# Optimization experiments

Measured on AMD Instinct MI355X. Metric: run time of the kernel, lower is better.

The kernel has to match this reference:

```python
import jax, jax.numpy as jnp
import numpy as np
from jax import lax

EPS = 1e-6
TANH_CLIP = 1.0 - 1e-5
FRECHET_ITERS = 10


def _sqnorm(x):
    return jnp.sum(x * x, axis=-1, keepdims=True)


def _norm(x):
    return jnp.sqrt(jnp.clip(_sqnorm(x), EPS))


def _lambda(x, c):
    # conformal factor lambda_x = 2 / (1 - c ||x||^2)
    return 2.0 / jnp.clip(1.0 - c * _sqnorm(x), EPS)


def mobius_add(x, y, c):
    x2 = _sqnorm(x)
    y2 = _sqnorm(y)
    xy = jnp.sum(x * y, axis=-1, keepdims=True)
    num = (1.0 + 2.0 * c * xy + c * y2) * x + (1.0 - c * x2) * y
    den = 1.0 + 2.0 * c * xy + (c * c) * x2 * y2
    return num / jnp.clip(den, EPS)


def expmap(x, u, c):
    sc = jnp.sqrt(c)
    un = _norm(u)
    second = jnp.tanh(sc * _lambda(x, c) * un / 2.0) * u / (sc * un)
    return mobius_add(x, second, c)


def logmap(x, y, c):
    sc = jnp.sqrt(c)
    m = mobius_add(-x, y, c)
    mn = _norm(m)
    t = jnp.arctanh(jnp.clip(sc * mn, 0.0, TANH_CLIP))
    return (2.0 / (sc * _lambda(x, c))) * t * m / mn


def exp0(u, c):
    sc = jnp.sqrt(c)
    un = _norm(u)
    return jnp.tanh(sc * un) * u / (sc * un)


def dist(x, y, c):
    sc = jnp.sqrt(c)
    mn = _norm(mobius_add(-x, y, c))
    return (2.0 / sc) * jnp.arctanh(jnp.clip(sc * mn, 0.0, TANH_CLIP))[..., 0]


def gyr(a, b, w, c):
    # gyr[a,b]w = -(a (+) b) (+) (a (+) (b (+) w))
    return mobius_add(-mobius_add(a, b, c), mobius_add(a, mobius_add(b, w, c), c), c)


def transp(x, y, u, c):
    # parallel transport x -> y:  (lam_x / lam_y) * gyr[y, -x] u
    return (_lambda(x, c) / _lambda(y, c)) * gyr(y, -x, u, c)


def frechet_mean(x, c):
    # Karcher fixed-point iteration: mu <- exp_mu(mean_i log_mu(x_i))
    m = jnp.mean(x, axis=0)  # (D,)
    max_norm = (1.0 - 1e-3) / jnp.sqrt(c)
    mn = _norm(m)[0]
    m = m * jnp.minimum(1.0, max_norm / mn)

    def step(mu, _):
        g = jnp.mean(logmap(mu, x, c), axis=0)
        return expmap(mu, g, c), None

    mu, _ = lax.scan(step, m, None, length=FRECHET_ITERS)
    return mu


def setup_inputs() -> dict:
    key = jax.random.key(0)
    k1, k2 = jax.random.split(key)
    B, S, D = 64, 256, 256
    K = jnp.float32(-1.2)
    sc = np.sqrt(1.2)
    x = jax.random.normal(k1, (B, S, D), dtype=jnp.float32)
    # project points strictly inside the Poincare ball of radius 1/sqrt(c)
    x = x / (1.0 + _norm(x)) * jnp.float32(0.7 / sc)
    mean_param = 0.01 * jax.random.normal(k2, (D,), dtype=jnp.float32)
    var_param = jnp.float32(1.0)
    return {"x": x, "K": K, "mean_param": mean_param, "var_param": var_param}


def reference(x, K, mean_param, var_param):
    c = -K  # positive ball curvature (K = -1.2)
    shapes = x.shape
    xf = x.reshape(-1, shapes[-1])  # (N, D)
    on_manifold = exp0(mean_param, c)          # (D,) target mean on manifold
    mu = frechet_mean(xf, c)                   # (D,) batch Frechet mean
    var = jnp.mean(dist(xf, mu, c) ** 2)       # Frechet variance (scalar)
    logm = transp(mu, on_manifold, logmap(mu, xf, c), c)  # (N, D)
    logm = jnp.sqrt(var_param / (var + 1e-6)) * logm
    out = expmap(on_manifold, logm, c)         # (N, D)
    return out.reshape(shapes)
```

## Files before the change

kernel.cpp:

```cpp
#include <hip/hip_runtime.h>
#include <math.h>
#include <string.h>

#define EPSF 1e-6f
#define TCLIP (1.0f - 1e-5f)
#define NPTS 16384
#define DDIM 256
#define NBLK 128
#define NTHR 1024
#define PPB 128
#define NWAVE 16
#define PPW 8
#define PSTR 260
#define FRECHET_ITERS_N 10

#define WS_PA 64
#define WS_PB (WS_PA + NBLK * PSTR)

__device__ __forceinline__ void st_pair_sc1(float* addr, float a, float b) {
    float2 f2 = make_float2(a, b);
    double dv; memcpy(&dv, &f2, 8);
    __hip_atomic_store((double*)addr, dv, __ATOMIC_RELAXED, __HIP_MEMORY_SCOPE_AGENT);
}
__device__ __forceinline__ float2 ld_pair_sc1(const float* addr) {
    double dv = __hip_atomic_load((const double*)addr, __ATOMIC_RELAXED, __HIP_MEMORY_SCOPE_AGENT);
    float2 f2; memcpy(&f2, &dv, 8);
    return f2;
}
__device__ __forceinline__ void st_f_sc1(float* addr, float v) {
    __hip_atomic_store(addr, v, __ATOMIC_RELAXED, __HIP_MEMORY_SCOPE_AGENT);
}
__device__ __forceinline__ void st_u_sc1(unsigned* addr, unsigned v) {
    __hip_atomic_store(addr, v, __ATOMIC_RELAXED, __HIP_MEMORY_SCOPE_AGENT);
}
__device__ __forceinline__ unsigned ld_u_sc1(const unsigned* addr) {
    return __hip_atomic_load(addr, __ATOMIC_RELAXED, __HIP_MEMORY_SCOPE_AGENT);
}

__device__ __forceinline__ float block_sum(float v) {
    __shared__ float s_bs[NWAVE];
    #pragma unroll
    for (int off = 32; off; off >>= 1) v += __shfl_xor(v, off);
    const int w = threadIdx.x >> 6, l = threadIdx.x & 63;
    __syncthreads();
    if (l == 0) s_bs[w] = v;
    __syncthreads();
    float s = 0.f;
    #pragma unroll
    for (int i = 0; i < NWAVE; ++i) s += s_bs[i];
    return s;
}

__device__ __forceinline__ void block_sum2(float& a, float& b) {
    __shared__ float sa2[NWAVE], sb2[NWAVE];
    #pragma unroll
    for (int off = 32; off; off >>= 1) { a += __shfl_xor(a, off); b += __shfl_xor(b, off); }
    const int w = threadIdx.x >> 6, l = threadIdx.x & 63;
    __syncthreads();
    if (l == 0) { sa2[w] = a; sb2[w] = b; }
    __syncthreads();
    a = 0.f; b = 0.f;
    #pragma unroll
    for (int i = 0; i < NWAVE; ++i) { a += sa2[i]; b += sb2[i]; }
}

__device__ __forceinline__ void block_sum3(float& a, float& b, float& cc) {
    __shared__ float sa3[NWAVE], sb3[NWAVE], sc3[NWAVE];
    #pragma unroll
    for (int off = 32; off; off >>= 1) {
        a += __shfl_xor(a, off); b += __shfl_xor(b, off); cc += __shfl_xor(cc, off);
    }
    const int w = threadIdx.x >> 6, l = threadIdx.x & 63;
    __syncthreads();
    if (l == 0) { sa3[w] = a; sb3[w] = b; sc3[w] = cc; }
    __syncthreads();
    a = 0.f; b = 0.f; cc = 0.f;
    #pragma unroll
    for (int i = 0; i < NWAVE; ++i) { a += sa3[i]; b += sb3[i]; cc += sc3[i]; }
}

__global__ void init_tags(float* ws) {
    int t = threadIdx.x;
    if (t < NBLK) {
        st_u_sc1((unsigned*)(ws + WS_PA + t * PSTR + 258), 0u);
        st_u_sc1((unsigned*)(ws + WS_PB + t * PSTR + 258), 0u);
    }
}

__global__ __launch_bounds__(NTHR, 1) void rbn_fused(
    const float* __restrict__ x, const float* __restrict__ Kp,
    const float* __restrict__ mean_param, const float* __restrict__ var_param,
    float* __restrict__ out, float* __restrict__ ws)
{
    const float c = -Kp[0];
    const float sc = sqrtf(c);
    const float N1 = 1.f / NPTS;
    const int t = threadIdx.x, lane = t & 63, wv = t >> 6;
    const int b = blockIdx.x;
    const int p0 = b * PPB;
    const float4* xr = ((const float4*)x) + p0 * 64;

    float* PA = ws + WS_PA;
    float* PB = ws + WS_PB;

    __shared__ float mu_s[DDIM], om_s[DDIM], g_s[DDIM];
    __shared__ float dpart[PPB * 65];
    __shared__ float dqr[PPB * 9];
    __shared__ float y2_s[PPB], e_s[PPB], d_s[PPB], w_s[PPB], sA_s[PPB], fx_s[PPB];
    __shared__ float pseg[NWAVE * DDIM];

    unsigned barno = 0;

    float4 xreg[PPW];
    #pragma unroll
    for (int i = 0; i < PPW; ++i)
        xreg[i] = xr[(wv * PPW + i) * 64 + lane];

    auto dot_rows = [&](float4 v4, float* dst, bool self) {
        #pragma unroll
        for (int i = 0; i < PPW; ++i) {
            float4 xv = xreg[i];
            float4 u4 = self ? xv : v4;
            dpart[(wv * PPW + i) * 65 + lane] =
                xv.x * u4.x + xv.y * u4.y + xv.z * u4.z + xv.w * u4.w;
        }
        __syncthreads();
        {
            int pl = t & 127, q = t >> 7;
            float s = 0.f;
            #pragma unroll
            for (int j = 0; j < 8; ++j) s += dpart[pl * 65 + q * 8 + j];
            dqr[pl * 9 + q] = s;
        }
        __syncthreads();
        if (t < PPB) {
            float s = 0.f;
            #pragma unroll
            for (int j = 0; j < 8; ++j) s += dqr[t * 9 + j];
            dst[t] = s;
        }
        __syncthreads();
    };

    auto wsum_rows = [&](const float* wgt, float* dstv) {
        float4 a = make_float4(0.f, 0.f, 0.f, 0.f);
        #pragma unroll
        for (int i = 0; i < PPW; ++i) {
            float w = wgt ? wgt[wv * PPW + i] : 1.f;
            a.x += w * xreg[i].x; a.y += w * xreg[i].y;
            a.z += w * xreg[i].z; a.w += w * xreg[i].w;
        }
        __syncthreads();
        ((float4*)(pseg + wv * DDIM))[lane] = a;
        __syncthreads();
        float s = 0.f;
        if (t < DDIM) {
            #pragma unroll
            for (int w = 0; w < NWAVE; ++w) s += pseg[w * DDIM + t];
        }
        float partner = __shfl_xor(s, 1);
        if (t < DDIM && !(t & 1))
            st_pair_sc1(dstv + t, s, partner);
    };

    auto publish = [&](float* buf) {
        __syncthreads();
        if (t == 0) st_u_sc1((unsigned*)(buf + b * PSTR + 258), barno);
    };
    auto wait_tags = [&](const float* buf) {
        if (t < NBLK) {
            const unsigned* tg = (const unsigned*)(buf + t * PSTR + 258);
            while (ld_u_sc1(tg) < barno)
                __builtin_amdgcn_s_sleep(1);
        }
        __syncthreads();
    };

    auto reduce128 = [&](const float* buf, float* dstv) {
        const int dg = t & 127, sg = t >> 7;
        float ax = 0.f, ay = 0.f;
        #pragma unroll
        for (int j = 0; j < 16; ++j) {
            float2 v = ld_pair_sc1(buf + (sg * 16 + j) * PSTR + 2 * dg);
            ax += v.x; ay += v.y;
        }
        __syncthreads();
        ((float2*)(pseg + sg * DDIM))[dg] = make_float2(ax, ay);
        __syncthreads();
        if (t < DDIM) {
            float s = 0.f;
            #pragma unroll
            for (int w = 0; w < 8; ++w) s += pseg[w * DDIM + t];
            dstv[t] = s;
        }
    };

    {
        float u = (t < DDIM) ? mean_param[t] : 0.f;
        float un2 = block_sum(u * u);
        float un = sqrtf(fmaxf(un2, EPSF));
        if (t < DDIM) om_s[t] = tanhf(sc * un) * u / (sc * un);
    }
    float om2;
    { float v = (t < DDIM) ? om_s[t] * om_s[t] : 0.f; om2 = block_sum(v); }

    dot_rows(make_float4(0.f, 0.f, 0.f, 0.f), y2_s, true);
    {
        float4 om4 = ((const float4*)om_s)[lane];
        dot_rows(om4, e_s, false);
    }

    ++barno;
    wsum_rows(nullptr, PA + b * PSTR);
    publish(PA);
    wait_tags(PA);

    float mu2;
    {
        reduce128(PA, g_s);
        float m = (t < DDIM) ? g_s[t] * N1 : 0.f;
        float mn2 = block_sum(m * m);
        float mn = sqrtf(fmaxf(mn2, EPSF));
        float maxn = (1.f - 1e-3f) / sc;
        float f = fminf(1.f, maxn / mn);
        if (t < DDIM) mu_s[t] = m * f;
        mu2 = f * f * mn2;
        __syncthreads();
    }

    for (int it = 0; it < FRECHET_ITERS_N; ++it) {
        float* buf = (it & 1) ? PA : PB;
        ++barno;
        {
            float4 mu4 = ((const float4*)mu_s)[lane];
            dot_rows(mu4, d_s, false);
        }
        if (t < PPB) {
            float y2 = y2_s[t], d = d_s[t];
            float P = 1.f - 2.f * c * d;
            float den = fmaxf(P + c * c * mu2 * y2, EPSF);
            float A = -(P + c * y2) / den;
            float B = (1.f - c * mu2) / den;
            float mn2 = fmaxf(A * A * mu2 + 2.f * A * B * d + B * B * y2, EPSF);
            float mn = sqrtf(mn2);
            float tt = atanhf(fminf(sc * mn, TCLIP));
            float s = (fmaxf(1.f - c * mu2, EPSF) / sc) * tt / mn;
            w_s[t] = s * B;
            sA_s[t] = s * A;
        }
        __syncthreads();
        wsum_rows(w_s, buf + b * PSTR);
        float sAl = (t < PPB) ? sA_s[t] : 0.f;
        float wdl = (t < PPB) ? w_s[t] * d_s[t] : 0.f;
        block_sum2(sAl, wdl);
        if (t == 0) st_pair_sc1(buf + b * PSTR + 256, sAl, wdl);
        publish(buf);
        wait_tags(buf);

        reduce128(buf, g_s);
        float vv  = (t < DDIM) ? g_s[t] * g_s[t] : 0.f;
        float2 sp = make_float2(0.f, 0.f);
        if (t < NBLK) sp = ld_pair_sc1(buf + t * PSTR + 256);
        float sAt = sp.x, wdt = sp.y;
        block_sum3(vv, sAt, wdt);
        float gn2 = N1 * N1 * (vv + 2.f * sAt * wdt + sAt * sAt * mu2);
        float mg  = N1 * (wdt + sAt * mu2);
        float un = sqrtf(fmaxf(gn2, EPSF));
        float lam = 2.f / fmaxf(1.f - c * mu2, EPSF);
        float k = tanhf(sc * lam * un * 0.5f) / (sc * un);
        float ms = k * mg;
        float s2 = k * k * gn2;
        float aa = 1.f + 2.f * c * ms + c * s2;
        float bb2 = 1.f - c * mu2;
        float den = fmaxf(1.f + 2.f * c * ms + c * c * mu2 * s2, EPSF);
        float cm = (aa + bb2 * k * N1 * sAt) / den;
        float cv = (bb2 * k * N1) / den;
        if (t < DDIM) mu_s[t] = cm * mu_s[t] + cv * g_s[t];
        mu2 = cm * cm * mu2 + 2.f * cm * cv * wdt + cv * cv * vv;
        __syncthreads();
    }

    float* vbuf = ((FRECHET_ITERS_N - 1) & 1) ? PB : PA;
    ++barno;
    {
        float4 mu4 = ((const float4*)mu_s)[lane];
        dot_rows(mu4, d_s, false);
    }
    if (t < PPB) {
        float y2 = y2_s[t], d = d_s[t];
        float P = 1.f - 2.f * c * d;
        float den = fmaxf(P + c * c * mu2 * y2, EPSF);
        float A = -(P + c * y2) / den;
        float B = (1.f - c * mu2) / den;
        float mn2 = fmaxf(A * A * mu2 + 2.f * A * B * d + B * B * y2, EPSF);
        float mn = sqrtf(mn2);
        float tt = atanhf(fminf(sc * mn, TCLIP));
        float dd = (2.f / sc) * tt;
        sA_s[t] = dd * dd;
    }
    __syncthreads();
    {
        float v = (t < PPB) ? sA_s[t] : 0.f;
        float tot = block_sum(v);
        if (t == 0) st_f_sc1(vbuf + b * PSTR + 256, tot);
    }
    publish(vbuf);
    wait_tags(vbuf);

    float va = (t < NBLK) ? __hip_atomic_load(vbuf + t * PSTR + 256,
                 __ATOMIC_RELAXED, __HIP_MEMORY_SCOPE_AGENT) : 0.f;
    float ob = (t < DDIM) ? om_s[t] * mu_s[t] : 0.f;
    block_sum2(va, ob);
    float var = va * N1;
    float gamma = sqrtf(var_param[0] / (var + 1e-6f));
    float omu = ob;

    const float Amu = fmaxf(1.f - c * mu2, EPSF);
    const float Aom = fmaxf(1.f - c * om2, EPSF);
    const float ratio = Aom / Amu;
    const float aq = 1.f - 2.f * c * omu + c * mu2;
    const float bq = 1.f - c * om2;
    const float dqv = fmaxf(1.f - 2.f * c * omu + c * c * om2 * mu2, EPSF);
    const float qo = aq / dqv, qm = -bq / dqv;
    const float q2 = qo * qo * om2 + 2.f * qo * qm * omu + qm * qm * mu2;
    const float lam_om = 2.f / Aom;

    if (t < PPB) {
        float y2 = y2_s[t], d = d_s[t], e = e_s[t];
        auto dotOm3 = [&](float po, float pm, float px) { return po * om2 + pm * omu + px * e; };
        auto dotMu3 = [&](float po, float pm, float px) { return po * omu + pm * mu2 + px * d; };
        auto sqn3 = [&](float po, float pm, float px) {
            return po * po * om2 + pm * pm * mu2 + px * px * y2
                 + 2.f * (po * pm * omu + po * px * e + pm * px * d);
        };

        float P = 1.f - 2.f * c * d;
        float den0 = fmaxf(P + c * c * mu2 * y2, EPSF);
        float A = -(P + c * y2) / den0;
        float B = (1.f - c * mu2) / den0;
        float mn2 = fmaxf(A * A * mu2 + 2.f * A * B * d + B * B * y2, EPSF);
        float mn = sqrtf(mn2);
        float tt = atanhf(fminf(sc * mn, TCLIP));
        float s = (fmaxf(1.f - c * mu2, EPSF) / sc) * tt / mn;
        float Um = s * A, Ux = s * B;

        float xy1 = -dotMu3(0.f, Um, Ux);
        float Y21 = sqn3(0.f, Um, Ux);
        float a1 = 1.f + 2.f * c * xy1 + c * Y21;
        float b1 = 1.f - c * mu2;
        float dn1 = fmaxf(1.f + 2.f * c * xy1 + c * c * mu2 * Y21, EPSF);
        float h1m = (-a1 + b1 * Um) / dn1;
        float h1x = (b1 * Ux) / dn1;

        float xy2 = dotOm3(0.f, h1m, h1x);
        float Y22 = sqn3(0.f, h1m, h1x);
        float a2 = 1.f + 2.f * c * xy2 + c * Y22;
        float b2 = 1.f - c * om2;
        float dn2 = fmaxf(1.f + 2.f * c * xy2 + c * c * om2 * Y22, EPSF);
        float h2o = a2 / dn2;
        float h2m = (b2 * h1m) / dn2;
        float h2x = (b2 * h1x) / dn2;

        float xy3 = -(qo * dotOm3(h2o, h2m, h2x) + qm * dotMu3(h2o, h2m, h2x));
        float Y23 = sqn3(h2o, h2m, h2x);
        float a3 = 1.f + 2.f * c * xy3 + c * Y23;
        float b3 = 1.f - c * q2;
        float dn3 = fmaxf(1.f + 2.f * c * xy3 + c * c * q2 * Y23, EPSF);
        float g2o = (-a3 * qo + b3 * h2o) / dn3;
        float g2m = (-a3 * qm + b3 * h2m) / dn3;
        float g2x = (b3 * h2x) / dn3;

        float k1 = ratio * gamma;
        float Lo = k1 * g2o, Lm = k1 * g2m, Lx = k1 * g2x;
        float un2 = sqn3(Lo, Lm, Lx);
        float un = sqrtf(fmaxf(un2, EPSF));
        float coef = tanhf(sc * lam_om * un * 0.5f) / (sc * un);
        float So = coef * Lo, Sm = coef * Lm, Sx = coef * Lx;
        float xy4 = dotOm3(So, Sm, Sx);
        float Y24 = coef * coef * un2;
        float a4 = 1.f + 2.f * c * xy4 + c * Y24;
        float b4 = 1.f - c * om2;
        float dn4 = fmaxf(1.f + 2.f * c * xy4 + c * c * om2 * Y24, EPSF);
        w_s[t]  = (a4 + b4 * So) / dn4;
        sA_s[t] = (b4 * Sm) / dn4;
        fx_s[t] = (b4 * Sx) / dn4;
    }
    __syncthreads();

    {
        float4 mu4f = ((const float4*)mu_s)[lane];
        float4 om4f = ((const float4*)om_s)[lane];
        #pragma unroll
        for (int i = 0; i < PPW; ++i) {
            int pl = wv * PPW + i;
            float fo = w_s[pl], fm = sA_s[pl], fx = fx_s[pl];
            float4 x4 = xreg[i];
            float4 o4;
            o4.x = fo * om4f.x + fm * mu4f.x + fx * x4.x;
            o4.y = fo * om4f.y + fm * mu4f.y + fx * x4.y;
            o4.z = fo * om4f.z + fm * mu4f.z + fx * x4.z;
            o4.w = fo * om4f.w + fm * mu4f.w + fx * x4.w;
            ((float4*)out)[(p0 + pl) * 64 + lane] = o4;
        }
    }
}

extern "C" void kernel_launch(void* const* d_in, const int* in_sizes, int n_in,
                              void* d_out, int out_size, void* d_ws, size_t ws_size,
                              hipStream_t stream) {
    const float* x = (const float*)d_in[0];
    const float* K = (const float*)d_in[1];
    const float* mean_param = (const float*)d_in[2];
    const float* var_param = (const float*)d_in[3];
    float* out = (float*)d_out;
    float* ws = (float*)d_ws;

    init_tags<<<1, 256, 0, stream>>>(ws);
    void* args[] = {(void*)&x, (void*)&K, (void*)&mean_param, (void*)&var_param,
                    (void*)&out, (void*)&ws};
    hipLaunchCooperativeKernel((const void*)rbn_fused, dim3(NBLK), dim3(NTHR),
                               args, 0, stream);
}
```

Measured before the change: 205.8 us.

## Overlap grid-barrier waits with local work and trim block-level syncs

```diff
diff --git a/kernel.cpp b/kernel.cpp
--- a/kernel.cpp
+++ b/kernel.cpp
@@ -30,6 +30,9 @@
 __device__ __forceinline__ void st_f_sc1(float* addr, float v) {
     __hip_atomic_store(addr, v, __ATOMIC_RELAXED, __HIP_MEMORY_SCOPE_AGENT);
 }
+__device__ __forceinline__ float ld_f_sc1(const float* addr) {
+    return __hip_atomic_load(addr, __ATOMIC_RELAXED, __HIP_MEMORY_SCOPE_AGENT);
+}
 __device__ __forceinline__ void st_u_sc1(unsigned* addr, unsigned v) {
     __hip_atomic_store(addr, v, __ATOMIC_RELAXED, __HIP_MEMORY_SCOPE_AGENT);
 }
@@ -49,34 +52,6 @@
     #pragma unroll
     for (int i = 0; i < NWAVE; ++i) s += s_bs[i];
     return s;
-}
-
-__device__ __forceinline__ void block_sum2(float& a, float& b) {
-    __shared__ float sa2[NWAVE], sb2[NWAVE];
-    #pragma unroll
-    for (int off = 32; off; off >>= 1) { a += __shfl_xor(a, off); b += __shfl_xor(b, off); }
-    const int w = threadIdx.x >> 6, l = threadIdx.x & 63;
-    __syncthreads();
-    if (l == 0) { sa2[w] = a; sb2[w] = b; }
-    __syncthreads();
-    a = 0.f; b = 0.f;
-    #pragma unroll
-    for (int i = 0; i < NWAVE; ++i) { a += sa2[i]; b += sb2[i]; }
-}
-
-__device__ __forceinline__ void block_sum3(float& a, float& b, float& cc) {
-    __shared__ float sa3[NWAVE], sb3[NWAVE], sc3[NWAVE];
-    #pragma unroll
-    for (int off = 32; off; off >>= 1) {
-        a += __shfl_xor(a, off); b += __shfl_xor(b, off); cc += __shfl_xor(cc, off);
-    }
-    const int w = threadIdx.x >> 6, l = threadIdx.x & 63;
-    __syncthreads();
-    if (l == 0) { sa3[w] = a; sb3[w] = b; sc3[w] = cc; }
-    __syncthreads();
-    a = 0.f; b = 0.f; cc = 0.f;
-    #pragma unroll
-    for (int i = 0; i < NWAVE; ++i) { a += sa3[i]; b += sb3[i]; cc += sc3[i]; }
 }
 
 __global__ void init_tags(float* ws) {
@@ -103,11 +78,12 @@
     float* PA = ws + WS_PA;
     float* PB = ws + WS_PB;
 
-    __shared__ float mu_s[DDIM], om_s[DDIM], g_s[DDIM];
+    __shared__ float mu_s[DDIM], om_s[DDIM];
     __shared__ float dpart[PPB * 65];
     __shared__ float dqr[PPB * 9];
     __shared__ float y2_s[PPB], e_s[PPB], d_s[PPB], w_s[PPB], sA_s[PPB], fx_s[PPB];
     __shared__ float pseg[NWAVE * DDIM];
+    __shared__ float part1[NWAVE], part2[NWAVE], part3[NWAVE];
 
     unsigned barno = 0;
 
@@ -116,58 +92,7 @@
     for (int i = 0; i < PPW; ++i)
         xreg[i] = xr[(wv * PPW + i) * 64 + lane];
 
-    auto dot_rows = [&](float4 v4, float* dst, bool self) {
-        #pragma unroll
-        for (int i = 0; i < PPW; ++i) {
-            float4 xv = xreg[i];
-            float4 u4 = self ? xv : v4;
-            dpart[(wv * PPW + i) * 65 + lane] =
-                xv.x * u4.x + xv.y * u4.y + xv.z * u4.z + xv.w * u4.w;
-        }
-        __syncthreads();
-        {
-            int pl = t & 127, q = t >> 7;
-            float s = 0.f;
-            #pragma unroll
-            for (int j = 0; j < 8; ++j) s += dpart[pl * 65 + q * 8 + j];
-            dqr[pl * 9 + q] = s;
-        }
-        __syncthreads();
-        if (t < PPB) {
-            float s = 0.f;
-            #pragma unroll
-            for (int j = 0; j < 8; ++j) s += dqr[t * 9 + j];
-            dst[t] = s;
-        }
-        __syncthreads();
-    };
-
-    auto wsum_rows = [&](const float* wgt, float* dstv) {
-        float4 a = make_float4(0.f, 0.f, 0.f, 0.f);
-        #pragma unroll
-        for (int i = 0; i < PPW; ++i) {
-            float w = wgt ? wgt[wv * PPW + i] : 1.f;
-            a.x += w * xreg[i].x; a.y += w * xreg[i].y;
-            a.z += w * xreg[i].z; a.w += w * xreg[i].w;
-        }
-        __syncthreads();
-        ((float4*)(pseg + wv * DDIM))[lane] = a;
-        __syncthreads();
-        float s = 0.f;
-        if (t < DDIM) {
-            #pragma unroll
-            for (int w = 0; w < NWAVE; ++w) s += pseg[w * DDIM + t];
-        }
-        float partner = __shfl_xor(s, 1);
-        if (t < DDIM && !(t & 1))
-            st_pair_sc1(dstv + t, s, partner);
-    };
-
-    auto publish = [&](float* buf) {
-        __syncthreads();
-        if (t == 0) st_u_sc1((unsigned*)(buf + b * PSTR + 258), barno);
-    };
-    auto wait_tags = [&](const float* buf) {
+    auto poll_tags = [&](const float* buf) {
         if (t < NBLK) {
             const unsigned* tg = (const unsigned*)(buf + t * PSTR + 258);
             while (ld_u_sc1(tg) < barno)
@@ -176,25 +101,6 @@
         __syncthreads();
     };
 
-    auto reduce128 = [&](const float* buf, float* dstv) {
-        const int dg = t & 127, sg = t >> 7;
-        float ax = 0.f, ay = 0.f;
-        #pragma unroll
-        for (int j = 0; j < 16; ++j) {
-            float2 v = ld_pair_sc1(buf + (sg * 16 + j) * PSTR + 2 * dg);
-            ax += v.x; ay += v.y;
-        }
-        __syncthreads();
-        ((float2*)(pseg + sg * DDIM))[dg] = make_float2(ax, ay);
-        __syncthreads();
-        if (t < DDIM) {
-            float s = 0.f;
-            #pragma unroll
-            for (int w = 0; w < 8; ++w) s += pseg[w * DDIM + t];
-            dstv[t] = s;
-        }
-    };
-
     {
         float u = (t < DDIM) ? mean_param[t] : 0.f;
         float un2 = block_sum(u * u);
@@ -204,22 +110,90 @@
     float om2;
     { float v = (t < DDIM) ? om_s[t] * om_s[t] : 0.f; om2 = block_sum(v); }
 
-    dot_rows(make_float4(0.f, 0.f, 0.f, 0.f), y2_s, true);
-    {
+    ++barno;
+    {
+        float4 a = make_float4(0.f, 0.f, 0.f, 0.f);
+        #pragma unroll
+        for (int i = 0; i < PPW; ++i) {
+            a.x += xreg[i].x; a.y += xreg[i].y; a.z += xreg[i].z; a.w += xreg[i].w;
+        }
+        __syncthreads();
+        ((float4*)(pseg + wv * DDIM))[lane] = a;
+        __syncthreads();
+        float s = 0.f;
+        if (t < DDIM) {
+            #pragma unroll
+            for (int w = 0; w < NWAVE; ++w) s += pseg[w * DDIM + t];
+        }
+        float partner = __shfl_xor(s, 1);
+        if (t < DDIM && !(t & 1)) st_pair_sc1(PA + b * PSTR + t, s, partner);
+        __syncthreads();
+        if (t == 0) st_u_sc1((unsigned*)(PA + b * PSTR + 258), barno);
+    }
+    {
+        #pragma unroll
+        for (int i = 0; i < PPW; ++i) {
+            float4 xv = xreg[i];
+            dpart[(wv * PPW + i) * 65 + lane] =
+                xv.x * xv.x + xv.y * xv.y + xv.z * xv.z + xv.w * xv.w;
+        }
+        __syncthreads();
+        { int pl = t & 127, q = t >> 7; float s = 0.f;
+          #pragma unroll
+          for (int j = 0; j < 8; ++j) s += dpart[pl * 65 + q * 8 + j];
+          dqr[pl * 9 + q] = s; }
+        __syncthreads();
+        if (t < PPB) { float s = 0.f;
+            #pragma unroll
+            for (int j = 0; j < 8; ++j) s += dqr[t * 9 + j];
+            y2_s[t] = s; }
+        __syncthreads();
         float4 om4 = ((const float4*)om_s)[lane];
-        dot_rows(om4, e_s, false);
-    }
-
-    ++barno;
-    wsum_rows(nullptr, PA + b * PSTR);
-    publish(PA);
-    wait_tags(PA);
+        #pragma unroll
+        for (int i = 0; i < PPW; ++i) {
+            float4 xv = xreg[i];
+            dpart[(wv * PPW + i) * 65 + lane] =
+                xv.x * om4.x + xv.y * om4.y + xv.z * om4.z + xv.w * om4.w;
+        }
+        __syncthreads();
+        { int pl = t & 127, q = t >> 7; float s = 0.f;
+          #pragma unroll
+          for (int j = 0; j < 8; ++j) s += dpart[pl * 65 + q * 8 + j];
+          dqr[pl * 9 + q] = s; }
+        __syncthreads();
+        if (t < PPB) { float s = 0.f;
+            #pragma unroll
+            for (int j = 0; j < 8; ++j) s += dqr[t * 9 + j];
+            e_s[t] = s; }
+    }
+    poll_tags(PA);
 
     float mu2;
     {
-        reduce128(PA, g_s);
-        float m = (t < DDIM) ? g_s[t] * N1 : 0.f;
-        float mn2 = block_sum(m * m);
+        const int dg = t & 127, sg = t >> 7;
+        float ax = 0.f, ay = 0.f;
+        #pragma unroll
+        for (int j = 0; j < 16; ++j) {
+            float2 v = ld_pair_sc1(PA + (sg * 16 + j) * PSTR + 2 * dg);
+            ax += v.x; ay += v.y;
+        }
+        __syncthreads();
+        ((float2*)(pseg + sg * DDIM))[dg] = make_float2(ax, ay);
+        __syncthreads();
+        float m = 0.f, mm = 0.f;
+        if (t < DDIM) {
+            float s = 0.f;
+            #pragma unroll
+            for (int w = 0; w < 8; ++w) s += pseg[w * DDIM + t];
+            m = s * N1; mm = m * m;
+        }
+        #pragma unroll
+        for (int off = 32; off; off >>= 1) mm += __shfl_xor(mm, off);
+        if (lane == 0) part1[wv] = mm;
+        __syncthreads();
+        float mn2 = 0.f;
+        #pragma unroll
+        for (int i = 0; i < NWAVE; ++i) mn2 += part1[i];
         float mn = sqrtf(fmaxf(mn2, EPSF));
         float maxn = (1.f - 1e-3f) / sc;
         float f = fminf(1.f, maxn / mn);
@@ -231,12 +205,25 @@
     for (int it = 0; it < FRECHET_ITERS_N; ++it) {
         float* buf = (it & 1) ? PA : PB;
         ++barno;
-        {
-            float4 mu4 = ((const float4*)mu_s)[lane];
-            dot_rows(mu4, d_s, false);
-        }
+        float4 mu4 = ((const float4*)mu_s)[lane];
+        #pragma unroll
+        for (int i = 0; i < PPW; ++i) {
+            float4 xv = xreg[i];
+            dpart[(wv * PPW + i) * 65 + lane] =
+                xv.x * mu4.x + xv.y * mu4.y + xv.z * mu4.z + xv.w * mu4.w;
+        }
+        __syncthreads();
+        { int pl = t & 127, q = t >> 7; float s = 0.f;
+          #pragma unroll
+          for (int j = 0; j < 8; ++j) s += dpart[pl * 65 + q * 8 + j];
+          dqr[pl * 9 + q] = s; }
+        __syncthreads();
+        float sAv = 0.f, wdv = 0.f;
         if (t < PPB) {
-            float y2 = y2_s[t], d = d_s[t];
+            float d = 0.f;
+            #pragma unroll
+            for (int j = 0; j < 8; ++j) d += dqr[t * 9 + j];
+            float y2 = y2_s[t];
             float P = 1.f - 2.f * c * d;
             float den = fmaxf(P + c * c * mu2 * y2, EPSF);
             float A = -(P + c * y2) / den;
@@ -245,26 +232,75 @@
             float mn = sqrtf(mn2);
             float tt = atanhf(fminf(sc * mn, TCLIP));
             float s = (fmaxf(1.f - c * mu2, EPSF) / sc) * tt / mn;
-            w_s[t] = s * B;
-            sA_s[t] = s * A;
-        }
-        __syncthreads();
-        wsum_rows(w_s, buf + b * PSTR);
-        float sAl = (t < PPB) ? sA_s[t] : 0.f;
-        float wdl = (t < PPB) ? w_s[t] * d_s[t] : 0.f;
-        block_sum2(sAl, wdl);
-        if (t == 0) st_pair_sc1(buf + b * PSTR + 256, sAl, wdl);
-        publish(buf);
-        wait_tags(buf);
-
-        reduce128(buf, g_s);
-        float vv  = (t < DDIM) ? g_s[t] * g_s[t] : 0.f;
+            float w = s * B;
+            w_s[t] = w;
+            sAv = s * A;
+            wdv = w * d;
+        }
+        __syncthreads();
+        {
+            float4 a = make_float4(0.f, 0.f, 0.f, 0.f);
+            #pragma unroll
+            for (int i = 0; i < PPW; ++i) {
+                float w = w_s[wv * PPW + i];
+                a.x += w * xreg[i].x; a.y += w * xreg[i].y;
+                a.z += w * xreg[i].z; a.w += w * xreg[i].w;
+            }
+            ((float4*)(pseg + wv * DDIM))[lane] = a;
+            #pragma unroll
+            for (int off = 32; off; off >>= 1) {
+                sAv += __shfl_xor(sAv, off); wdv += __shfl_xor(wdv, off);
+            }
+            if (lane == 0) { part1[wv] = sAv; part2[wv] = wdv; }
+        }
+        __syncthreads();
+        {
+            float s = 0.f;
+            if (t < DDIM) {
+                #pragma unroll
+                for (int w = 0; w < NWAVE; ++w) s += pseg[w * DDIM + t];
+            }
+            float partner = __shfl_xor(s, 1);
+            if (t < DDIM && !(t & 1)) st_pair_sc1(buf + b * PSTR + t, s, partner);
+            if (t == 0) {
+                float sa = 0.f, wd = 0.f;
+                #pragma unroll
+                for (int i = 0; i < NWAVE; ++i) { sa += part1[i]; wd += part2[i]; }
+                st_pair_sc1(buf + b * PSTR + 256, sa, wd);
+            }
+        }
+        __syncthreads();
+        if (t == 0) st_u_sc1((unsigned*)(buf + b * PSTR + 258), barno);
+        poll_tags(buf);
+        const int dg = t & 127, sg = t >> 7;
+        float ax = 0.f, ay = 0.f;
+        #pragma unroll
+        for (int j = 0; j < 16; ++j) {
+            float2 v = ld_pair_sc1(buf + (sg * 16 + j) * PSTR + 2 * dg);
+            ax += v.x; ay += v.y;
+        }
         float2 sp = make_float2(0.f, 0.f);
         if (t < NBLK) sp = ld_pair_sc1(buf + t * PSTR + 256);
+        ((float2*)(pseg + sg * DDIM))[dg] = make_float2(ax, ay);
+        __syncthreads();
+        float g = 0.f, vvv = 0.f;
+        if (t < DDIM) {
+            #pragma unroll
+            for (int w = 0; w < 8; ++w) g += pseg[w * DDIM + t];
+            vvv = g * g;
+        }
         float sAt = sp.x, wdt = sp.y;
-        block_sum3(vv, sAt, wdt);
-        float gn2 = N1 * N1 * (vv + 2.f * sAt * wdt + sAt * sAt * mu2);
-        float mg  = N1 * (wdt + sAt * mu2);
+        #pragma unroll
+        for (int off = 32; off; off >>= 1) {
+            vvv += __shfl_xor(vvv, off); sAt += __shfl_xor(sAt, off); wdt += __shfl_xor(wdt, off);
+        }
+        if (lane == 0) { part1[wv] = vvv; part2[wv] = sAt; part3[wv] = wdt; }
+        __syncthreads();
+        float vv = 0.f, sa = 0.f, wd = 0.f;
+        #pragma unroll
+        for (int i = 0; i < NWAVE; ++i) { vv += part1[i]; sa += part2[i]; wd += part3[i]; }
+        float gn2 = N1 * N1 * (vv + 2.f * sa * wd + sa * sa * mu2);
+        float mg  = N1 * (wd + sa * mu2);
         float un = sqrtf(fmaxf(gn2, EPSF));
         float lam = 2.f / fmaxf(1.f - c * mu2, EPSF);
         float k = tanhf(sc * lam * un * 0.5f) / (sc * un);
@@ -273,10 +309,10 @@
         float aa = 1.f + 2.f * c * ms + c * s2;
         float bb2 = 1.f - c * mu2;
         float den = fmaxf(1.f + 2.f * c * ms + c * c * mu2 * s2, EPSF);
-        float cm = (aa + bb2 * k * N1 * sAt) / den;
+        float cm = (aa + bb2 * k * N1 * sa) / den;
         float cv = (bb2 * k * N1) / den;
-        if (t < DDIM) mu_s[t] = cm * mu_s[t] + cv * g_s[t];
-        mu2 = cm * cm * mu2 + 2.f * cm * cv * wdt + cv * cv * vv;
+        if (t < DDIM) mu_s[t] = cm * mu_s[t] + cv * g;
+        mu2 = cm * cm * mu2 + 2.f * cm * cv * wd + cv * cv * vv;
         __syncthreads();
     }
 
@@ -284,36 +320,54 @@
     ++barno;
     {
         float4 mu4 = ((const float4*)mu_s)[lane];
-        dot_rows(mu4, d_s, false);
-    }
-    if (t < PPB) {
-        float y2 = y2_s[t], d = d_s[t];
-        float P = 1.f - 2.f * c * d;
-        float den = fmaxf(P + c * c * mu2 * y2, EPSF);
-        float A = -(P + c * y2) / den;
-        float B = (1.f - c * mu2) / den;
-        float mn2 = fmaxf(A * A * mu2 + 2.f * A * B * d + B * B * y2, EPSF);
-        float mn = sqrtf(mn2);
-        float tt = atanhf(fminf(sc * mn, TCLIP));
-        float dd = (2.f / sc) * tt;
-        sA_s[t] = dd * dd;
-    }
-    __syncthreads();
-    {
-        float v = (t < PPB) ? sA_s[t] : 0.f;
-        float tot = block_sum(v);
-        if (t == 0) st_f_sc1(vbuf + b * PSTR + 256, tot);
-    }
-    publish(vbuf);
-    wait_tags(vbuf);
-
-    float va = (t < NBLK) ? __hip_atomic_load(vbuf + t * PSTR + 256,
-                 __ATOMIC_RELAXED, __HIP_MEMORY_SCOPE_AGENT) : 0.f;
-    float ob = (t < DDIM) ? om_s[t] * mu_s[t] : 0.f;
-    block_sum2(va, ob);
-    float var = va * N1;
-    float gamma = sqrtf(var_param[0] / (var + 1e-6f));
-    float omu = ob;
+        #pragma unroll
+        for (int i = 0; i < PPW; ++i) {
+            float4 xv = xreg[i];
+            dpart[(wv * PPW + i) * 65 + lane] =
+                xv.x * mu4.x + xv.y * mu4.y + xv.z * mu4.z + xv.w * mu4.w;
+        }
+        __syncthreads();
+        { int pl = t & 127, q = t >> 7; float s = 0.f;
+          #pragma unroll
+          for (int j = 0; j < 8; ++j) s += dpart[pl * 65 + q * 8 + j];
+          dqr[pl * 9 + q] = s; }
+        __syncthreads();
+        float vval = 0.f;
+        if (t < PPB) {
+            float d = 0.f;
+            #pragma unroll
+            for (int j = 0; j < 8; ++j) d += dqr[t * 9 + j];
+            d_s[t] = d;
+            float y2 = y2_s[t];
+            float P = 1.f - 2.f * c * d;
+            float den = fmaxf(P + c * c * mu2 * y2, EPSF);
+            float A = -(P + c * y2) / den;
+            float B = (1.f - c * mu2) / den;
+            float mn2 = fmaxf(A * A * mu2 + 2.f * A * B * d + B * B * y2, EPSF);
+            float mn = sqrtf(mn2);
+            float tt = atanhf(fminf(sc * mn, TCLIP));
+            float dd = (2.f / sc) * tt;
+            vval = dd * dd;
+        }
+        float ov = (t < DDIM) ? om_s[t] * mu_s[t] : 0.f;
+        #pragma unroll
+        for (int off = 32; off; off >>= 1) {
+            vval += __shfl_xor(vval, off); ov += __shfl_xor(ov, off);
+        }
+        if (lane == 0) { part1[wv] = vval; part2[wv] = ov; }
+        __syncthreads();
+        if (t == 0) {
+            float tot = 0.f;
+            #pragma unroll
+            for (int i = 0; i < NWAVE; ++i) tot += part1[i];
+            st_f_sc1(vbuf + b * PSTR + 256, tot);
+        }
+        __syncthreads();
+        if (t == 0) st_u_sc1((unsigned*)(vbuf + b * PSTR + 258), barno);
+    }
+    float omu = 0.f;
+    #pragma unroll
+    for (int i = 0; i < NWAVE; ++i) omu += part2[i];
 
     const float Amu = fmaxf(1.f - c * mu2, EPSF);
     const float Aom = fmaxf(1.f - c * om2, EPSF);
@@ -333,7 +387,6 @@
             return po * po * om2 + pm * pm * mu2 + px * px * y2
                  + 2.f * (po * pm * omu + po * px * e + pm * px * d);
         };
-
         float P = 1.f - 2.f * c * d;
         float den0 = fmaxf(P + c * c * mu2 * y2, EPSF);
         float A = -(P + c * y2) / den0;
@@ -366,17 +419,34 @@
         float a3 = 1.f + 2.f * c * xy3 + c * Y23;
         float b3 = 1.f - c * q2;
         float dn3 = fmaxf(1.f + 2.f * c * xy3 + c * c * q2 * Y23, EPSF);
-        float g2o = (-a3 * qo + b3 * h2o) / dn3;
-        float g2m = (-a3 * qm + b3 * h2m) / dn3;
-        float g2x = (b3 * h2x) / dn3;
-
+        w_s[t]  = (-a3 * qo + b3 * h2o) / dn3;
+        sA_s[t] = (-a3 * qm + b3 * h2m) / dn3;
+        fx_s[t] = (b3 * h2x) / dn3;
+    }
+    poll_tags(vbuf);
+
+    float va = (t < NBLK) ? ld_f_sc1(vbuf + t * PSTR + 256) : 0.f;
+    #pragma unroll
+    for (int off = 32; off; off >>= 1) va += __shfl_xor(va, off);
+    if (lane == 0) part1[wv] = va;
+    __syncthreads();
+    float vsum = 0.f;
+    #pragma unroll
+    for (int i = 0; i < NWAVE; ++i) vsum += part1[i];
+    float var = vsum * N1;
+    float gamma = sqrtf(var_param[0] / (var + 1e-6f));
+
+    if (t < PPB) {
+        float y2 = y2_s[t], d = d_s[t], e = e_s[t];
+        float g2o = w_s[t], g2m = sA_s[t], g2x = fx_s[t];
         float k1 = ratio * gamma;
         float Lo = k1 * g2o, Lm = k1 * g2m, Lx = k1 * g2x;
-        float un2 = sqn3(Lo, Lm, Lx);
+        float un2 = Lo * Lo * om2 + Lm * Lm * mu2 + Lx * Lx * y2
+                  + 2.f * (Lo * Lm * omu + Lo * Lx * e + Lm * Lx * d);
         float un = sqrtf(fmaxf(un2, EPSF));
         float coef = tanhf(sc * lam_om * un * 0.5f) / (sc * un);
         float So = coef * Lo, Sm = coef * Lm, Sx = coef * Lx;
-        float xy4 = dotOm3(So, Sm, Sx);
+        float xy4 = So * om2 + Sm * omu + Sx * e;
         float Y24 = coef * coef * un2;
         float a4 = 1.f + 2.f * c * xy4 + c * Y24;
         float b4 = 1.f - c * om2;
```

After: 188.1 us. 1.09x faster.
